# Optimization experiments

Hardware: AMD Instinct MI355X
Metric: run time of the kernel (lower is better)

The kernel has to match this reference:

```python
import jax, jax.numpy as jnp
import numpy as np

B, N, K = 128, 512, 6      # graphs, nodes per graph, kNN neighbors
IN_FEAT, POS_DIM, H = 128, 3, 256
NB = B * N                  # total nodes
EPS_BN = 1e-5


def setup_inputs() -> dict:
    key = jax.random.key(0)
    ks = jax.random.split(key, 32)
    inp = {
        "x": jax.random.normal(ks[0], (NB, IN_FEAT), dtype=jnp.float32),
        "pos": jax.random.normal(ks[1], (NB, POS_DIM), dtype=jnp.float32) * 5.0,
    }
    d_in = IN_FEAT + POS_DIM
    def lin(k, fi, fo):
        s = 1.0 / np.sqrt(fi)
        return jax.random.uniform(k, (fi, fo), jnp.float32, -s, s)
    # GCN layers
    inp["W1"] = lin(ks[2], d_in, H); inp["b1"] = jnp.zeros((H,), jnp.float32)
    inp["W2"] = lin(ks[3], H, H);    inp["b2"] = jnp.zeros((H,), jnp.float32)
    inp["W3"] = lin(ks[4], H, H);    inp["b3"] = jnp.zeros((H,), jnp.float32)
    # BatchNorm (eval mode: running stats)
    for i, km, kv in [(1, ks[5], ks[6]), (2, ks[7], ks[8]), (3, ks[9], ks[10])]:
        inp[f"g{i}"]  = jnp.ones((H,), jnp.float32)
        inp[f"be{i}"] = jnp.zeros((H,), jnp.float32)
        inp[f"m{i}"]  = jax.random.normal(km, (H,), jnp.float32) * 0.1
        inp[f"v{i}"]  = jax.random.uniform(kv, (H,), jnp.float32, 0.5, 1.5)
    # attention gate, heads
    inp["gate_w"] = lin(ks[11], H, 1); inp["gate_b"] = jnp.zeros((1,), jnp.float32)
    inp["aff_w"]  = lin(ks[12], H, 1); inp["aff_b"]  = jnp.zeros((1,), jnp.float32)
    inp["rl_w1"]  = lin(ks[13], H, H); inp["rl_b1"]  = jnp.zeros((H,), jnp.float32)
    inp["rl_w2"]  = lin(ks[14], H, POS_DIM); inp["rl_b2"] = jnp.zeros((POS_DIM,), jnp.float32)
    return inp


def _knn_edges(pos):
    # torch_geometric knn_graph semantics: per-graph k nearest neighbors,
    # no self loops, edges (neighbor -> node).  batch = repeat(arange(B), N).
    p = pos.reshape(B, N, POS_DIM)
    sq = jnp.sum(p * p, axis=-1)                                  # [B,N]
    d2 = sq[:, :, None] + sq[:, None, :] - 2.0 * jnp.einsum("bnd,bmd->bnm", p, p)
    d2 = jnp.where(jnp.eye(N, dtype=bool)[None], jnp.inf, d2)     # exclude self
    _, idx = jax.lax.top_k(-d2, K)                                # [B,N,K] local nbr ids
    offs = (jnp.arange(B) * N)[:, None, None]
    src = (idx + offs).reshape(-1)                                # neighbor (source)
    dst = jnp.repeat(jnp.arange(NB), K)                           # target node
    return src, dst


def _gcn(h, W, b, src, dst):
    # GCNConv: add self loops, symmetric norm D^-1/2 (A+I) D^-1/2
    hw = h @ W                                                    # [NB,H]
    deg = jax.ops.segment_sum(jnp.ones_like(dst, jnp.float32), dst, num_segments=NB) + 1.0
    dis = jax.lax.rsqrt(deg)
    norm = dis[src] * dis[dst]                                    # [E]
    agg = jax.ops.segment_sum(hw[src] * norm[:, None], dst, num_segments=NB)
    agg = agg + hw * (1.0 / deg)[:, None]                          # self loop term
    return agg + b


def _bn(h, g, be, m, v):
    return (h - m) * (g * jax.lax.rsqrt(v + EPS_BN)) + be


def reference(x, pos, W1, b1, W2, b2, W3, b3,
              g1, be1, m1, v1, g2, be2, m2, v2, g3, be3, m3, v3,
              gate_w, gate_b, aff_w, aff_b, rl_w1, rl_b1, rl_w2, rl_b2):
    src, dst = _knn_edges(pos)
    h = jnp.concatenate([x, pos], axis=1)                          # [NB, in_feat+3]
    h = jax.nn.relu(_bn(_gcn(h, W1, b1, src, dst), g1, be1, m1, v1))
    h = jax.nn.relu(_bn(_gcn(h, W2, b2, src, dst), g2, be2, m2, v2))
    h = jax.nn.relu(_bn(_gcn(h, W3, b3, src, dst), g3, be3, m3, v3))
    # (dropout is identity in eval mode)
    gate = jax.nn.relu(h @ gate_w + gate_b)[:, 0]                  # [NB]
    attn = jax.nn.softmax(gate.reshape(B, N), axis=1)              # scatter_softmax over batch
    gemb = jnp.einsum("bn,bnh->bh", attn, h.reshape(B, N, H))      # scatter_add of weighted x
    affinity = gemb @ aff_w + aff_b                                # [B,1]
    pose = jax.nn.relu(gemb @ rl_w1 + rl_b1) @ rl_w2 + rl_b2        # [B,3]
    return affinity, pose
```

## Files before the change

kernel.cpp:

```cpp
#include <hip/hip_runtime.h>
#include <hip/hip_bf16.h>
#include <math.h>
#include <float.h>

#define NBG 128
#define NND 512
#define KNN 6
#define NB_TOT (NBG*NND)
#define HF 256
#define NSTEP1 5

typedef short bf16x8 __attribute__((ext_vector_type(8)));
typedef float f32x4 __attribute__((ext_vector_type(4)));

__device__ __forceinline__ int swzoff(int row, int kbyte) {
    return (row*64 + kbyte) ^ (((row>>1)&3)<<4);
}

__device__ __forceinline__ void split_store(const float* v, char* hi_p, char* lo_p) {
    bf16x8 hi, lo;
    #pragma unroll
    for (int j = 0; j < 8; ++j) {
        __hip_bfloat16 h = __float2bfloat16(v[j]);
        float hf = __bfloat162float(h);
        __hip_bfloat16 l = __float2bfloat16(v[j] - hf);
        hi[j] = *(short*)&h;
        lo[j] = *(short*)&l;
    }
    *(bf16x8*)hi_p = hi;
    *(bf16x8*)lo_p = lo;
}

__device__ __forceinline__ int xcd_swz(int bid, int grid) {
    return (bid & 7) * (grid >> 3) + (bid >> 3);
}

__global__ __launch_bounds__(256) void knn_kernel(const float* __restrict__ pos,
                                                  unsigned short* __restrict__ nbr)
{
    const int blk = blockIdx.x;
    const int g = blk >> 3;
    const int chunk = (blk & 7) * 64;
    const int tid = threadIdx.x;
    const int node = chunk + (tid >> 2);
    const int sub = tid & 3;

    __shared__ float4 p4[NND + (NND>>6)];
    const float* pg = pos + (size_t)g * NND * 3;
    for (int n = tid; n < NND; n += 256) {
        float x = pg[n*3+0], y = pg[n*3+1], z = pg[n*3+2];
        p4[n + (n>>6)] = make_float4(x, y, z, x*x + y*y + z*z);
    }
    __syncthreads();

    const float4 pi = p4[node + (node>>6)];
    const float m2x = -2.0f*pi.x, m2y = -2.0f*pi.y, m2z = -2.0f*pi.z;

    float bdA[KNN], bdB[KNN]; int biA[KNN], biB[KNN];
    #pragma unroll
    for (int q = 0; q < KNN; ++q) {
        bdA[q] = FLT_MAX; biA[q] = 0x7fffffff;
        bdB[q] = FLT_MAX; biB[q] = 0x7fffffff;
    }

    const int j0 = sub * 128;
    const float4* baseA = &p4[sub*130];
    const float4* baseB = &p4[sub*130 + 65];

    #pragma unroll 2
    for (int t = 0; t < 64; ++t) {
        int ja = j0 + t, jb = j0 + 64 + t;
        float4 pa = baseA[t];
        float4 pb = baseB[t];
        float da = fmaf(m2z, pa.z, fmaf(m2y, pa.y, fmaf(m2x, pa.x, pa.w)));
        float db = fmaf(m2z, pb.z, fmaf(m2y, pb.y, fmaf(m2x, pb.x, pb.w)));
        da = (ja == node) ? FLT_MAX : da;
        db = (jb == node) ? FLT_MAX : db;
        float ca = da; int ia = ja;
        float cb = db; int ib = jb;
        #pragma unroll
        for (int q = 0; q < KNN; ++q) {
            bool sa = ca < bdA[q];
            float t1 = sa ? ca : bdA[q]; float t2 = sa ? bdA[q] : ca;
            int   t3 = sa ? ia : biA[q]; int   t4 = sa ? biA[q] : ia;
            bdA[q] = t1; ca = t2; biA[q] = t3; ia = t4;
            bool sb = cb < bdB[q];
            float u1 = sb ? cb : bdB[q]; float u2 = sb ? bdB[q] : cb;
            int   u3 = sb ? ib : biB[q]; int   u4 = sb ? biB[q] : ib;
            bdB[q] = u1; cb = u2; biB[q] = u3; ib = u4;
        }
    }

    float ld[KNN]; int li[KNN];
    #pragma unroll
    for (int q = 0; q < KNN; ++q) {
        float ad = bdA[q], xd = bdB[KNN-1-q];
        int   ai = biA[q], xi = biB[KNN-1-q];
        bool t = (ad < xd) || (ad == xd && ai < xi);
        ld[q] = t ? ad : xd;
        li[q] = t ? ai : xi;
    }
    #pragma unroll
    for (int pass = 0; pass < KNN-1; ++pass)
        #pragma unroll
        for (int a = 0; a < KNN-1-pass; ++a) {
            int b = a+1;
            bool sw = (ld[b] < ld[a]) || (ld[b] == ld[a] && li[b] < li[a]);
            float td = sw ? ld[b] : ld[a]; float ud = sw ? ld[a] : ld[b];
            int   ti = sw ? li[b] : li[a]; int   ui = sw ? li[a] : li[b];
            ld[a] = td; li[a] = ti; ld[b] = ud; li[b] = ui;
        }

    #pragma unroll
    for (int mi = 0; mi < 2; ++mi) {
        const int mask = 1 << mi;
        float od[KNN]; int oi[KNN];
        #pragma unroll
        for (int q = 0; q < KNN; ++q) {
            od[q] = __shfl_xor(ld[q], mask);
            oi[q] = __shfl_xor(li[q], mask);
        }
        #pragma unroll
        for (int q = 0; q < KNN; ++q) {
            float ad = ld[q], xd = od[KNN-1-q];
            int   ai = li[q], xi = oi[KNN-1-q];
            bool t = (ad < xd) || (ad == xd && ai < xi);
            ld[q] = t ? ad : xd;
            li[q] = t ? ai : xi;
        }
        #pragma unroll
        for (int pass = 0; pass < KNN-1; ++pass)
            #pragma unroll
            for (int a = 0; a < KNN-1-pass; ++a) {
                int b = a+1;
                bool sw = (ld[b] < ld[a]) || (ld[b] == ld[a] && li[b] < li[a]);
                float td = sw ? ld[b] : ld[a]; float ud = sw ? ld[a] : ld[b];
                int   ti = sw ? li[b] : li[a]; int   ui = sw ? li[a] : li[b];
                ld[a] = td; li[a] = ti; ld[b] = ud; li[b] = ui;
            }
    }

    if (sub == 0) {
        int base = (g*NND + node)*KNN;
        #pragma unroll
        for (int q = 0; q < KNN; ++q) nbr[base+q] = (unsigned short)li[q];
    }
}

__global__ __launch_bounds__(256) void prew_all(
    const float* __restrict__ W1, const float* __restrict__ W2,
    const float* __restrict__ W3,
    char* __restrict__ I1, char* __restrict__ I2, char* __restrict__ I3)
{
    int b = blockIdx.x;
    const float* W; char* img; int K, nstep;
    if (b < 20)      { W = W1; img = I1; K = 131; nstep = 5; }
    else if (b < 52) { W = W2; img = I2; K = 256; nstep = 8; b -= 20; }
    else             { W = W3; img = I3; K = 256; nstep = 8; b -= 52; }
    int gid = b*256 + threadIdx.x;
    int per_nb = nstep*512;
    int nb = gid / per_nb;
    int r  = gid - nb*per_nb;
    int step = r >> 9;
    int r2 = r & 511;
    int cl = r2 >> 2;
    int kc = (r2 & 3) * 8;
    float v[8];
    #pragma unroll
    for (int j = 0; j < 8; ++j) {
        int gk = step*32 + kc + j;
        v[j] = (gk < K) ? W[(size_t)gk*256 + nb*128 + cl] : 0.f;
    }
    char* base = img + (size_t)nb*nstep*16384 + (size_t)step*16384;
    int off = swzoff(cl, kc*2);
    split_store(v, base + off, base + 8192 + off);
}

__global__ __launch_bounds__(256) void agg_first(const float* __restrict__ x,
                                                 const float* __restrict__ pos,
                                                 const unsigned short* __restrict__ nbr,
                                                 char* __restrict__ Aimg)
{
    int gid = xcd_swz(blockIdx.x, gridDim.x)*256 + threadIdx.x;
    int i = gid / 20, ch = gid - i*20;
    const float rs = 1.0f/sqrtf(7.0f);
    const float c1 = rs*rs, c2 = 1.0f/7.0f;
    const int gbase = i & ~(NND-1);
    float v[8];
    if (ch < 16) {
        int jn[KNN];
        #pragma unroll
        for (int q = 0; q < KNN; ++q) jn[q] = gbase + nbr[i*KNN+q];
        const float4* x4 = (const float4*)x;
        int c4 = ch*2;
        float4 s0 = x4[(size_t)i*32 + c4], s1 = x4[(size_t)i*32 + c4 + 1];
        float a0=0,a1=0,a2=0,a3=0,b0=0,b1=0,b2=0,b3=0;
        #pragma unroll
        for (int q = 0; q < KNN; ++q) {
            float4 t0 = x4[(size_t)jn[q]*32 + c4];
            float4 t1 = x4[(size_t)jn[q]*32 + c4 + 1];
            a0+=t0.x; a1+=t0.y; a2+=t0.z; a3+=t0.w;
            b0+=t1.x; b1+=t1.y; b2+=t1.z; b3+=t1.w;
        }
        v[0]=a0*c1+s0.x*c2; v[1]=a1*c1+s0.y*c2; v[2]=a2*c1+s0.z*c2; v[3]=a3*c1+s0.w*c2;
        v[4]=b0*c1+s1.x*c2; v[5]=b1*c1+s1.y*c2; v[6]=b2*c1+s1.z*c2; v[7]=b3*c1+s1.w*c2;
    } else if (ch == 16) {
        int jn[KNN];
        #pragma unroll
        for (int q = 0; q < KNN; ++q) jn[q] = gbase + nbr[i*KNN+q];
        float ax=0, ay=0, az=0;
        #pragma unroll
        for (int q = 0; q < KNN; ++q) {
            ax += pos[(size_t)jn[q]*3+0];
            ay += pos[(size_t)jn[q]*3+1];
            az += pos[(size_t)jn[q]*3+2];
        }
        v[0] = ax*c1 + pos[(size_t)i*3+0]*c2;
        v[1] = ay*c1 + pos[(size_t)i*3+1]*c2;
        v[2] = az*c1 + pos[(size_t)i*3+2]*c2;
        v[3]=v[4]=v[5]=v[6]=v[7]=0.f;
    } else {
        #pragma unroll
        for (int j = 0; j < 8; ++j) v[j] = 0.f;
    }
    int mb = i >> 7, row = i & 127, step = ch >> 2, kbyte = (ch & 3)*16;
    char* base = Aimg + (size_t)mb*(NSTEP1*16384) + (size_t)step*16384;
    int off = swzoff(row, kbyte);
    split_store(v, base + off, base + 8192 + off);
}

__global__ __launch_bounds__(256,4) void gemm_mfma(
    const char* __restrict__ Aimg, const char* __restrict__ Wimg, int nstep,
    const float* __restrict__ bias,
    const float* __restrict__ gam, const float* __restrict__ bet,
    const float* __restrict__ mu,  const float* __restrict__ var,
    float* __restrict__ out)
{
    __shared__ uint4 lds4[34816/16];
    char* lds  = (char*)lds4;
    char* Alds = lds;
    char* Wlds = lds + 16384;
    float* scs = (float*)(lds + 32768);
    float* shs = scs + 256;
    const int tid = threadIdx.x;
    const int lane = tid & 63, wave = tid >> 6;
    const int wm = wave >> 1, wn = wave & 1;
    const int mblk = blockIdx.x, nblk = blockIdx.y;

    if (tid < 256) {
        float s = gam[tid] / sqrtf(var[tid] + 1e-5f);
        scs[tid] = s;
        shs[tid] = bet[tid] + (bias[tid] - mu[tid]) * s;
    }

    const char* Ab = Aimg + (size_t)mblk * nstep * 16384;
    const char* Wb = Wimg + (size_t)nblk * nstep * 16384;

    const char* gbase; char* lbase;
    int soff;
    if (wave < 2) { gbase = Ab;  lbase = Alds; soff = wave*8192; }
    else          { gbase = Wb;  lbase = Wlds; soff = (wave-2)*8192; }

    f32x4 acc[4][4];
    #pragma unroll
    for (int m = 0; m < 4; ++m)
        #pragma unroll
        for (int n = 0; n < 4; ++n) acc[m][n] = (f32x4){0.f,0.f,0.f,0.f};

    for (int s = 0; s < nstep; ++s) {
        #pragma unroll
        for (int i = 0; i < 8; ++i) {
            int off = soff + i*1024;
            __builtin_amdgcn_global_load_lds(
                (const __attribute__((address_space(1))) void*)(gbase + (size_t)s*16384 + off + lane*16),
                (__attribute__((address_space(3))) void*)(lbase + off), 16, 0, 0);
        }
        __syncthreads();
        const int kb = (lane >> 4) * 16;
        bf16x8 ah[4], al[4];
        #pragma unroll
        for (int m = 0; m < 4; ++m) {
            int row = wm*64 + m*16 + (lane & 15);
            int off = swzoff(row, kb);
            ah[m] = *(const bf16x8*)(Alds + off);
            al[m] = *(const bf16x8*)(Alds + 8192 + off);
        }
        #pragma unroll
        for (int n = 0; n < 4; ++n) {
            int col = wn*64 + n*16 + (lane & 15);
            int off = swzoff(col, kb);
            bf16x8 bh = *(const bf16x8*)(Wlds + off);
            bf16x8 bl = *(const bf16x8*)(Wlds + 8192 + off);
            #pragma unroll
            for (int m = 0; m < 4; ++m) {
                acc[m][n] = __builtin_amdgcn_mfma_f32_16x16x32_bf16(ah[m], bh, acc[m][n], 0, 0, 0);
                acc[m][n] = __builtin_amdgcn_mfma_f32_16x16x32_bf16(al[m], bh, acc[m][n], 0, 0, 0);
                acc[m][n] = __builtin_amdgcn_mfma_f32_16x16x32_bf16(ah[m], bl, acc[m][n], 0, 0, 0);
            }
        }
        __syncthreads();
    }

    #pragma unroll
    for (int n = 0; n < 4; ++n) {
        int c = nblk*128 + wn*64 + n*16 + (lane & 15);
        float sc = scs[c], sh = shs[c];
        #pragma unroll
        for (int m = 0; m < 4; ++m) {
            int r0 = mblk*128 + wm*64 + m*16 + (lane >> 4)*4;
            #pragma unroll
            for (int q = 0; q < 4; ++q) {
                float v = acc[m][n][q]*sc + sh;
                out[(size_t)(r0+q)*256 + c] = fmaxf(v, 0.f);
            }
        }
    }
}

__global__ __launch_bounds__(256,3) void gcn_fused(
    const float* __restrict__ hin,
    const unsigned short* __restrict__ nbr,
    const char* __restrict__ Wimg,
    const float* __restrict__ bias,
    const float* __restrict__ gam, const float* __restrict__ bet,
    const float* __restrict__ mu,  const float* __restrict__ var,
    float* __restrict__ hout)
{
    __shared__ uint4 lds4[43008/16];
    char* Alds = (char*)lds4;
    char* Wlds = (char*)lds4 + 8192;
    float* scs = (float*)((char*)lds4 + 40960);
    float* shs = scs + 256;
    const int tid = threadIdx.x;
    const int lane = tid & 63, wave = tid >> 6;
    const int wn = wave;
    const int mblk = xcd_swz(blockIdx.x, gridDim.x);

    {
        float s = gam[tid] / sqrtf(var[tid] + 1e-5f);
        scs[tid] = s;
        shs[tid] = bet[tid] + (bias[tid] - mu[tid]) * s;
    }

    const int arow = tid >> 2, ch = tid & 3;
    const int gnode = mblk*64 + arow;
    const int gb = gnode & ~(NND-1);
    int jn[KNN];
    #pragma unroll
    for (int q = 0; q < KNN; ++q) jn[q] = gb + nbr[gnode*KNN + q];
    const float rs = 1.0f/sqrtf(7.0f);
    const float c1 = rs*rs, c2 = 1.0f/7.0f;
    const int aoff = swzoff(arow, ch*16);
    const float4* h4 = (const float4*)hin;

    f32x4 acc[4][4];
    #pragma unroll
    for (int m = 0; m < 4; ++m)
        #pragma unroll
        for (int n = 0; n < 4; ++n) acc[m][n] = (f32x4){0.f,0.f,0.f,0.f};

    float4 pf[14];
    {
        const int fb = ch*2;
        #pragma unroll
        for (int q = 0; q < KNN; ++q) {
            pf[2*q]   = h4[(size_t)jn[q]*64 + fb];
            pf[2*q+1] = h4[(size_t)jn[q]*64 + fb + 1];
        }
        pf[12] = h4[(size_t)gnode*64 + fb];
        pf[13] = h4[(size_t)gnode*64 + fb + 1];
    }

    for (int s = 0; s < 8; ++s) {
        {
            float a0 = pf[0].x + pf[2].x + pf[4].x + pf[6].x + pf[8].x + pf[10].x;
            float a1 = pf[0].y + pf[2].y + pf[4].y + pf[6].y + pf[8].y + pf[10].y;
            float a2 = pf[0].z + pf[2].z + pf[4].z + pf[6].z + pf[8].z + pf[10].z;
            float a3 = pf[0].w + pf[2].w + pf[4].w + pf[6].w + pf[8].w + pf[10].w;
            float b0 = pf[1].x + pf[3].x + pf[5].x + pf[7].x + pf[9].x + pf[11].x;
            float b1 = pf[1].y + pf[3].y + pf[5].y + pf[7].y + pf[9].y + pf[11].y;
            float b2 = pf[1].z + pf[3].z + pf[5].z + pf[7].z + pf[9].z + pf[11].z;
            float b3 = pf[1].w + pf[3].w + pf[5].w + pf[7].w + pf[9].w + pf[11].w;
            float v[8];
            v[0]=a0*c1+pf[12].x*c2; v[1]=a1*c1+pf[12].y*c2;
            v[2]=a2*c1+pf[12].z*c2; v[3]=a3*c1+pf[12].w*c2;
            v[4]=b0*c1+pf[13].x*c2; v[5]=b1*c1+pf[13].y*c2;
            v[6]=b2*c1+pf[13].z*c2; v[7]=b3*c1+pf[13].w*c2;
            split_store(v, Alds + aoff, Alds + 4096 + aoff);
        }
        #pragma unroll
        for (int i = 0; i < 8; ++i) {
            int woff = i*4096 + wave*1024;
            size_t srcoff = (woff < 16384) ? ((size_t)s*16384 + woff)
                                           : ((size_t)(8+s)*16384 + (woff - 16384));
            __builtin_amdgcn_global_load_lds(
                (const __attribute__((address_space(1))) void*)(Wimg + srcoff + lane*16),
                (__attribute__((address_space(3))) void*)(Wlds + woff), 16, 0, 0);
        }
        __syncthreads();
        if (s < 7) {
            const int fb = (s+1)*8 + ch*2;
            #pragma unroll
            for (int q = 0; q < KNN; ++q) {
                pf[2*q]   = h4[(size_t)jn[q]*64 + fb];
                pf[2*q+1] = h4[(size_t)jn[q]*64 + fb + 1];
            }
            pf[12] = h4[(size_t)gnode*64 + fb];
            pf[13] = h4[(size_t)gnode*64 + fb + 1];
        }
        const int kb = (lane >> 4) * 16;
        bf16x8 ah[4], al[4];
        #pragma unroll
        for (int m = 0; m < 4; ++m) {
            int o = swzoff(m*16 + (lane & 15), kb);
            ah[m] = *(const bf16x8*)(Alds + o);
            al[m] = *(const bf16x8*)(Alds + 4096 + o);
        }
        const char* wreg = Wlds + (wn >> 1)*16384;
        #pragma unroll
        for (int n = 0; n < 4; ++n) {
            int cl = (wn & 1)*64 + n*16 + (lane & 15);
            int o = swzoff(cl, kb);
            bf16x8 bh = *(const bf16x8*)(wreg + o);
            bf16x8 bl = *(const bf16x8*)(wreg + 8192 + o);
            #pragma unroll
            for (int m = 0; m < 4; ++m) {
                acc[m][n] = __builtin_amdgcn_mfma_f32_16x16x32_bf16(ah[m], bh, acc[m][n], 0, 0, 0);
                acc[m][n] = __builtin_amdgcn_mfma_f32_16x16x32_bf16(al[m], bh, acc[m][n], 0, 0, 0);
                acc[m][n] = __builtin_amdgcn_mfma_f32_16x16x32_bf16(ah[m], bl, acc[m][n], 0, 0, 0);
            }
        }
        __syncthreads();
    }

    #pragma unroll
    for (int n = 0; n < 4; ++n) {
        int c = wn*64 + n*16 + (lane & 15);
        float sc = scs[c], sh = shs[c];
        #pragma unroll
        for (int m = 0; m < 4; ++m) {
            int r0 = mblk*64 + m*16 + (lane >> 4)*4;
            #pragma unroll
            for (int q = 0; q < 4; ++q) {
                float v = acc[m][n][q]*sc + sh;
                hout[(size_t)(r0+q)*256 + c] = fmaxf(v, 0.f);
            }
        }
    }
}

__global__ __launch_bounds__(256) void gate_kernel(const float* __restrict__ h3,
                                                   const float* __restrict__ gate_w,
                                                   const float* __restrict__ gate_b,
                                                   float* __restrict__ gate)
{
    const int lane = threadIdx.x & 63;
    const int gw = (blockIdx.x*256 + threadIdx.x) >> 6;
    float4 w4 = ((const float4*)gate_w)[lane];
    float gb = gate_b[0];
    #pragma unroll
    for (int it = 0; it < 4; ++it) {
        int r = gw + it*8192;
        float4 v = ((const float4*)(h3 + (size_t)r*HF))[lane];
        float s = v.x*w4.x + v.y*w4.y + v.z*w4.z + v.w*w4.w;
        #pragma unroll
        for (int o = 32; o > 0; o >>= 1) s += __shfl_xor(s, o, 64);
        if (lane == 0) gate[r] = fmaxf(s + gb, 0.f);
    }
}

__device__ __forceinline__ float blk_sum256(float v, volatile float* red)
{
    #pragma unroll
    for (int o = 32; o > 0; o >>= 1) v += __shfl_xor(v, o, 64);
    __syncthreads();
    if ((threadIdx.x & 63) == 0) red[threadIdx.x >> 6] = v;
    __syncthreads();
    return (red[0] + red[1]) + (red[2] + red[3]);
}

__global__ __launch_bounds__(256) void gemb_kernel(const float* __restrict__ h3,
                                                   const float* __restrict__ gate,
                                                   float* __restrict__ gembp)
{
    const int g = blockIdx.x, s = blockIdx.y;
    const int tid = threadIdx.x, lane = tid & 63, w = tid >> 6;
    __shared__ float at[128];
    __shared__ float red4[4][HF];
    __shared__ float red[4];

    float g0 = gate[g*NND + tid];
    float g1 = gate[g*NND + 256 + tid];
    float m = fmaxf(g0, g1);
    #pragma unroll
    for (int o = 32; o > 0; o >>= 1) m = fmaxf(m, __shfl_xor(m, o, 64));
    if ((tid & 63) == 0) red[tid >> 6] = m;
    __syncthreads();
    m = fmaxf(fmaxf(red[0], red[1]), fmaxf(red[2], red[3]));
    float S = blk_sum256(expf(g0 - m) + expf(g1 - m), red);
    if (tid < 128) at[tid] = expf(gate[g*NND + s*128 + tid] - m) / S;
    __syncthreads();

    const float* hb = h3 + (size_t)(g*NND + s*128 + w*32) * HF;
    float4 acc = make_float4(0.f, 0.f, 0.f, 0.f);
    #pragma unroll 4
    for (int n = 0; n < 32; ++n) {
        float a = at[w*32 + n];
        float4 v = ((const float4*)(hb + (size_t)n*HF))[lane];
        acc.x = fmaf(a, v.x, acc.x); acc.y = fmaf(a, v.y, acc.y);
        acc.z = fmaf(a, v.z, acc.z); acc.w = fmaf(a, v.w, acc.w);
    }
    *(float4*)&red4[w][lane*4] = acc;
    __syncthreads();
    if (tid < HF) {
        float sum = (red4[0][tid] + red4[1][tid]) + (red4[2][tid] + red4[3][tid]);
        gembp[((size_t)s*NBG + g)*HF + tid] = sum;
    }
}

__global__ __launch_bounds__(256) void heads_kernel(
    const float* __restrict__ gembp,
    const float* __restrict__ aff_w,  const float* __restrict__ aff_b,
    const float* __restrict__ rl_w1,  const float* __restrict__ rl_b1,
    const float* __restrict__ rl_w2,  const float* __restrict__ rl_b2,
    float* __restrict__ out)
{
    int g = blockIdx.x, tid = threadIdx.x;
    __shared__ float gemb[HF];
    __shared__ float red[4];
    float acc = (gembp[((size_t)0*NBG + g)*HF + tid] + gembp[((size_t)1*NBG + g)*HF + tid])
              + (gembp[((size_t)2*NBG + g)*HF + tid] + gembp[((size_t)3*NBG + g)*HF + tid]);
    gemb[tid] = acc;
    __syncthreads();

    float sa = blk_sum256(acc * aff_w[tid], red);
    if (tid == 0) out[g] = sa + aff_b[0];

    float t = rl_b1[tid];
    #pragma unroll 4
    for (int k2 = 0; k2 < HF; ++k2)
        t = fmaf(gemb[k2], rl_w1[(size_t)k2*HF + tid], t);
    t = fmaxf(t, 0.f);
    float s0 = blk_sum256(t * rl_w2[(size_t)tid*3 + 0], red);
    if (tid == 0) out[128 + g*3 + 0] = s0 + rl_b2[0];
    float s1 = blk_sum256(t * rl_w2[(size_t)tid*3 + 1], red);
    if (tid == 0) out[128 + g*3 + 1] = s1 + rl_b2[1];
    float s2 = blk_sum256(t * rl_w2[(size_t)tid*3 + 2], red);
    if (tid == 0) out[128 + g*3 + 2] = s2 + rl_b2[2];
}

extern "C" void kernel_launch(void* const* d_in, const int* in_sizes, int n_in,
                              void* d_out, int out_size, void* d_ws, size_t ws_size,
                              hipStream_t stream)
{
    const float* x      = (const float*)d_in[0];
    const float* pos    = (const float*)d_in[1];
    const float* W1     = (const float*)d_in[2];
    const float* b1     = (const float*)d_in[3];
    const float* W2     = (const float*)d_in[4];
    const float* b2     = (const float*)d_in[5];
    const float* W3     = (const float*)d_in[6];
    const float* b3     = (const float*)d_in[7];
    const float* g1     = (const float*)d_in[8];
    const float* be1    = (const float*)d_in[9];
    const float* m1     = (const float*)d_in[10];
    const float* v1     = (const float*)d_in[11];
    const float* g2     = (const float*)d_in[12];
    const float* be2    = (const float*)d_in[13];
    const float* m2     = (const float*)d_in[14];
    const float* v2     = (const float*)d_in[15];
    const float* g3     = (const float*)d_in[16];
    const float* be3    = (const float*)d_in[17];
    const float* m3     = (const float*)d_in[18];
    const float* v3     = (const float*)d_in[19];
    const float* gate_w = (const float*)d_in[20];
    const float* gate_b = (const float*)d_in[21];
    const float* aff_w  = (const float*)d_in[22];
    const float* aff_b  = (const float*)d_in[23];
    const float* rl_w1  = (const float*)d_in[24];
    const float* rl_b1  = (const float*)d_in[25];
    const float* rl_w2  = (const float*)d_in[26];
    const float* rl_b2  = (const float*)d_in[27];
    float* out = (float*)d_out;

    char* wsb = (char*)d_ws;
    unsigned short* nbr = (unsigned short*)wsb;
    char* Wimg1 = wsb + 786432;
    char* Wimg2 = Wimg1 + (size_t)2*NSTEP1*16384;
    char* Wimg3 = Wimg2 + (size_t)2*8*16384;
    float* h_a  = (float*)(Wimg3 + (size_t)2*8*16384);
    char* regB  = (char*)(h_a + (size_t)NB_TOT*HF);
    char*  Aimg  = regB;
    float* h_b   = (float*)regB;
    float* gate  = (float*)regB;
    float* gembp = (float*)(regB + (size_t)NB_TOT*4);

    knn_kernel<<<NBG*8, 256, 0, stream>>>(pos, nbr);
    prew_all<<<84, 256, 0, stream>>>(W1, W2, W3, Wimg1, Wimg2, Wimg3);

    agg_first<<<(NB_TOT*20)/256, 256, 0, stream>>>(x, pos, nbr, Aimg);
    gemm_mfma<<<dim3(NB_TOT/128, 2), 256, 0, stream>>>(Aimg, Wimg1, NSTEP1,
        b1, g1, be1, m1, v1, h_a);
    gcn_fused<<<NB_TOT/64, 256, 0, stream>>>(h_a, nbr, Wimg2,
        b2, g2, be2, m2, v2, h_b);
    gcn_fused<<<NB_TOT/64, 256, 0, stream>>>(h_b, nbr, Wimg3,
        b3, g3, be3, m3, v3, h_a);

    gate_kernel<<<2048, 256, 0, stream>>>(h_a, gate_w, gate_b, gate);
    gemb_kernel<<<dim3(NBG, 4), 256, 0, stream>>>(h_a, gate, gembp);
    heads_kernel<<<NBG, 256, 0, stream>>>(gembp, aff_w, aff_b,
                                          rl_w1, rl_b1, rl_w2, rl_b2, out);
}
```

Before: 215.2 us.

## Load GCN weight fragments directly into registers and double-buffer A tile

```diff
diff --git a/kernel.cpp b/kernel.cpp
--- a/kernel.cpp
+++ b/kernel.cpp
@@ -317,7 +317,7 @@
     }
 }
 
-__global__ __launch_bounds__(256,3) void gcn_fused(
+__global__ __launch_bounds__(256,2) void gcn_fused(
     const float* __restrict__ hin,
     const unsigned short* __restrict__ nbr,
     const char* __restrict__ Wimg,
@@ -326,10 +326,9 @@
     const float* __restrict__ mu,  const float* __restrict__ var,
     float* __restrict__ hout)
 {
-    __shared__ uint4 lds4[43008/16];
+    __shared__ uint4 lds4[18944/16];
     char* Alds = (char*)lds4;
-    char* Wlds = (char*)lds4 + 8192;
-    float* scs = (float*)((char*)lds4 + 40960);
+    float* scs = (float*)((char*)lds4 + 16384);
     float* shs = scs + 256;
     const int tid = threadIdx.x;
     const int lane = tid & 63, wave = tid >> 6;
@@ -353,6 +352,13 @@
     const int aoff = swzoff(arow, ch*16);
     const float4* h4 = (const float4*)hin;
 
+    const int kb = (lane >> 4) * 16;
+    const char* wbase = Wimg + (size_t)(wn >> 1) * 8 * 16384;
+    int wo[4];
+    #pragma unroll
+    for (int n = 0; n < 4; ++n)
+        wo[n] = swzoff((wn & 1)*64 + n*16 + (lane & 15), kb);
+
     f32x4 acc[4][4];
     #pragma unroll
     for (int m = 0; m < 4; ++m)
@@ -360,18 +366,25 @@
         for (int n = 0; n < 4; ++n) acc[m][n] = (f32x4){0.f,0.f,0.f,0.f};
 
     float4 pf[14];
+    bf16x8 wfh[2][4], wfl[2][4];
     {
-        const int fb = ch*2;
         #pragma unroll
         for (int q = 0; q < KNN; ++q) {
-            pf[2*q]   = h4[(size_t)jn[q]*64 + fb];
-            pf[2*q+1] = h4[(size_t)jn[q]*64 + fb + 1];
-        }
-        pf[12] = h4[(size_t)gnode*64 + fb];
-        pf[13] = h4[(size_t)gnode*64 + fb + 1];
-    }
-
+            pf[2*q]   = h4[(size_t)jn[q]*64 + ch*2];
+            pf[2*q+1] = h4[(size_t)jn[q]*64 + ch*2 + 1];
+        }
+        pf[12] = h4[(size_t)gnode*64 + ch*2];
+        pf[13] = h4[(size_t)gnode*64 + ch*2 + 1];
+        #pragma unroll
+        for (int n = 0; n < 4; ++n) {
+            wfh[0][n] = *(const bf16x8*)(wbase + wo[n]);
+            wfl[0][n] = *(const bf16x8*)(wbase + 8192 + wo[n]);
+        }
+    }
+
+    #pragma unroll
     for (int s = 0; s < 8; ++s) {
+        char* Ab = Alds + (s & 1)*8192;
         {
             float a0 = pf[0].x + pf[2].x + pf[4].x + pf[6].x + pf[8].x + pf[10].x;
             float a1 = pf[0].y + pf[2].y + pf[4].y + pf[6].y + pf[8].y + pf[10].y;
@@ -386,16 +399,7 @@
             v[2]=a2*c1+pf[12].z*c2; v[3]=a3*c1+pf[12].w*c2;
             v[4]=b0*c1+pf[13].x*c2; v[5]=b1*c1+pf[13].y*c2;
             v[6]=b2*c1+pf[13].z*c2; v[7]=b3*c1+pf[13].w*c2;
-            split_store(v, Alds + aoff, Alds + 4096 + aoff);
-        }
-        #pragma unroll
-        for (int i = 0; i < 8; ++i) {
-            int woff = i*4096 + wave*1024;
-            size_t srcoff = (woff < 16384) ? ((size_t)s*16384 + woff)
-                                           : ((size_t)(8+s)*16384 + (woff - 16384));
-            __builtin_amdgcn_global_load_lds(
-                (const __attribute__((address_space(1))) void*)(Wimg + srcoff + lane*16),
-                (__attribute__((address_space(3))) void*)(Wlds + woff), 16, 0, 0);
+            split_store(v, Ab + aoff, Ab + 4096 + aoff);
         }
         __syncthreads();
         if (s < 7) {
@@ -407,22 +411,24 @@
             }
             pf[12] = h4[(size_t)gnode*64 + fb];
             pf[13] = h4[(size_t)gnode*64 + fb + 1];
-        }
-        const int kb = (lane >> 4) * 16;
+            const char* plane = wbase + (size_t)(s+1)*16384;
+            #pragma unroll
+            for (int n = 0; n < 4; ++n) {
+                wfh[(s+1)&1][n] = *(const bf16x8*)(plane + wo[n]);
+                wfl[(s+1)&1][n] = *(const bf16x8*)(plane + 8192 + wo[n]);
+            }
+        }
         bf16x8 ah[4], al[4];
         #pragma unroll
         for (int m = 0; m < 4; ++m) {
             int o = swzoff(m*16 + (lane & 15), kb);
-            ah[m] = *(const bf16x8*)(Alds + o);
-            al[m] = *(const bf16x8*)(Alds + 4096 + o);
-        }
-        const char* wreg = Wlds + (wn >> 1)*16384;
+            ah[m] = *(const bf16x8*)(Ab + o);
+            al[m] = *(const bf16x8*)(Ab + 4096 + o);
+        }
         #pragma unroll
         for (int n = 0; n < 4; ++n) {
-            int cl = (wn & 1)*64 + n*16 + (lane & 15);
-            int o = swzoff(cl, kb);
-            bf16x8 bh = *(const bf16x8*)(wreg + o);
-            bf16x8 bl = *(const bf16x8*)(wreg + 8192 + o);
+            bf16x8 bh = wfh[s & 1][n];
+            bf16x8 bl = wfl[s & 1][n];
             #pragma unroll
             for (int m = 0; m < 4; ++m) {
                 acc[m][n] = __builtin_amdgcn_mfma_f32_16x16x32_bf16(ah[m], bh, acc[m][n], 0, 0, 0);
@@ -430,7 +436,6 @@
                 acc[m][n] = __builtin_amdgcn_mfma_f32_16x16x32_bf16(ah[m], bl, acc[m][n], 0, 0, 0);
             }
         }
-        __syncthreads();
     }
 
     #pragma unroll
```

Result: slower. 232.0 us (+7.8%).
